# Performance work log

Measured on AMD Instinct MI355X. Metric: run time of the kernel, lower is better.

The kernel has to match this reference:

```python
import jax, jax.numpy as jnp
import numpy as np

N_NODES = 50000
N_EDGES = 1000000
D_NODE = 64
D_EDGE = 64


def setup_inputs() -> dict:
    key = jax.random.key(0)
    ks = jax.random.split(key, 12)
    d, de = D_NODE, D_EDGE
    din = 2 * d + de
    s = lambda f_in: 1.0 / np.sqrt(f_in)
    return {
        "node_feat": jax.random.normal(ks[0], (N_NODES, d), jnp.float32),
        "edge_src": jax.random.randint(ks[1], (N_EDGES,), 0, N_NODES, jnp.int32),
        "edge_dst": jax.random.randint(ks[2], (N_EDGES,), 0, N_NODES, jnp.int32),
        "edge_feat": jax.random.normal(ks[3], (N_EDGES, de), jnp.float32),
        # msg_mlp: Linear(din,d) -> SiLU -> Linear(d,d)
        "W_m1": jax.random.uniform(ks[4], (din, d), jnp.float32, -s(din), s(din)),
        "b_m1": jax.random.uniform(ks[5], (d,), jnp.float32, -s(din), s(din)),
        "W_m2": jax.random.uniform(ks[6], (d, d), jnp.float32, -s(d), s(d)),
        "b_m2": jax.random.uniform(ks[7], (d,), jnp.float32, -s(d), s(d)),
        # update_mlp: Linear(d,d) -> SiLU -> Linear(d,d)
        "W_u1": jax.random.uniform(ks[8], (d, d), jnp.float32, -s(d), s(d)),
        "b_u1": jax.random.uniform(ks[9], (d,), jnp.float32, -s(d), s(d)),
        "W_u2": jax.random.uniform(ks[10], (d, d), jnp.float32, -s(d), s(d)),
        "b_u2": jax.random.uniform(ks[11], (d,), jnp.float32, -s(d), s(d)),
        # LayerNorm params
        "ln_gamma": jnp.ones((d,), jnp.float32),
        "ln_beta": jnp.zeros((d,), jnp.float32),
    }


def _layer_norm(x, gamma, beta, eps=1e-5):
    mu = jnp.mean(x, axis=-1, keepdims=True)
    var = jnp.var(x, axis=-1, keepdims=True)
    return (x - mu) * jax.lax.rsqrt(var + eps) * gamma + beta


def reference(node_feat, edge_src, edge_dst, edge_feat,
              W_m1, b_m1, W_m2, b_m2, W_u1, b_u1, W_u2, b_u2,
              ln_gamma, ln_beta):
    # gather endpoint features per edge: [E, 2d+de]
    msg_input = jnp.concatenate(
        [node_feat[edge_src], node_feat[edge_dst], edge_feat], axis=-1)
    h = jax.nn.silu(msg_input @ W_m1 + b_m1)
    messages = h @ W_m2 + b_m2                      # [E, d]
    aggregated = jax.ops.segment_sum(messages, edge_dst,
                                     num_segments=node_feat.shape[0])
    upd = jax.nn.silu(aggregated @ W_u1 + b_u1) @ W_u2 + b_u2
    return _layer_norm(node_feat + upd, ln_gamma, ln_beta)
```

## Files before the change

kernel.cpp:

```cpp
#include <hip/hip_runtime.h>
#include <stdint.h>

typedef __bf16 bf16;
typedef __attribute__((ext_vector_type(8))) bf16 bf16x8;
typedef __attribute__((ext_vector_type(4))) float f32x4;

#define D 64
#define EPW 32

__device__ __forceinline__ float silu_f(float x) {
    return x / (1.0f + __expf(-x));
}

__global__ void cvt_hist_kernel(const float* __restrict__ nf, bf16* __restrict__ nfb,
                                const int* __restrict__ edst, int* __restrict__ cnt,
                                int total8, int E) {
    const int i = blockIdx.x * blockDim.x + threadIdx.x;
    if (i < total8) {
        f32x4 a = ((const f32x4*)nf)[i*2], b = ((const f32x4*)nf)[i*2 + 1];
        bf16x8 v;
        #pragma unroll
        for (int k = 0; k < 4; ++k) { v[k] = (bf16)a[k]; v[4+k] = (bf16)b[k]; }
        ((bf16x8*)nfb)[i] = v;
    }
    const int stride = gridDim.x * blockDim.x;
    for (int e = i; e < E; e += stride)
        atomicAdd(&cnt[edst[e]], 1);
}

__global__ void scan_part_kernel(const int* __restrict__ cnt, int* __restrict__ part, int N) {
    __shared__ int red[256];
    const int t = threadIdx.x, idx = blockIdx.x * 256 + t;
    red[t] = (idx < N) ? cnt[idx] : 0;
    __syncthreads();
    for (int off = 128; off; off >>= 1) {
        if (t < off) red[t] += red[t + off];
        __syncthreads();
    }
    if (t == 0) part[blockIdx.x] = red[0];
}

__global__ void scan_base_kernel(int* __restrict__ part, int nblk) {
    __shared__ int sc[256];
    const int t = threadIdx.x;
    const int v = (t < nblk) ? part[t] : 0;
    sc[t] = v;
    __syncthreads();
    for (int off = 1; off < 256; off <<= 1) {
        int u = (t >= off) ? sc[t - off] : 0;
        __syncthreads();
        sc[t] += u;
        __syncthreads();
    }
    part[t] = sc[t] - v;
}

__global__ void scan_fin_kernel(const int* __restrict__ cnt, const int* __restrict__ part,
                                int* __restrict__ cur, float* __restrict__ outz, int N) {
    __shared__ int sc[256];
    const int t = threadIdx.x, idx = blockIdx.x * 256 + t;
    const int v = (idx < N) ? cnt[idx] : 0;
    sc[t] = v;
    __syncthreads();
    for (int off = 1; off < 256; off <<= 1) {
        int u = (t >= off) ? sc[t - off] : 0;
        __syncthreads();
        sc[t] += u;
        __syncthreads();
    }
    if (idx < N) {
        cur[idx] = sc[t] - v + part[blockIdx.x];
        f32x4 z = {0.f, 0.f, 0.f, 0.f};
        float* o = outz + (size_t)idx * D;
        #pragma unroll
        for (int i = 0; i < 16; ++i) ((f32x4*)o)[i] = z;
    }
}

__global__ void scatter_kernel(const int* __restrict__ esrc, const int* __restrict__ edst,
                               int* __restrict__ cur, int4* __restrict__ sde, int E) {
    const int stride = gridDim.x * blockDim.x;
    for (int e = blockIdx.x * blockDim.x + threadIdx.x; e < E; e += stride) {
        const int d = edst[e];
        const int pos = atomicAdd(&cur[d], 1);
        sde[pos] = make_int4(esrc[e], d, e, 0);
    }
}

__launch_bounds__(512, 4)
__global__ void mp_edge_sorted_kernel(
    const bf16* __restrict__ nfb,
    const int4* __restrict__ sde,
    const float* __restrict__ efeat,
    const float* __restrict__ W1, const float* __restrict__ b1,
    const float* __restrict__ W2, const float* __restrict__ b2,
    float* __restrict__ agg,
    int E)
{
    __shared__ __align__(16) bf16 W1f[6*4*64*8];
    __shared__ __align__(16) bf16 W2f[2*4*64*8];
    __shared__ __align__(16) bf16 HM[8][32*72];
    __shared__ float b1s[D], b2s[D];

    const int t    = threadIdx.x;
    const int lane = t & 63;
    const int w    = t >> 6;
    const int g    = lane >> 4;
    const int c    = lane & 15;

    for (int idx = t; idx < 6*4*64; idx += 512) {
        int l = idx & 63, nt = (idx >> 6) & 3, ks = idx >> 8;
        int k0 = ks*32 + (l >> 4)*8, col = nt*16 + (l & 15);
        bf16x8 v;
        #pragma unroll
        for (int i = 0; i < 8; ++i) v[i] = (bf16)W1[(k0 + i)*D + col];
        *(bf16x8*)&W1f[idx*8] = v;
    }
    for (int idx = t; idx < 2*4*64; idx += 512) {
        int l = idx & 63, nt = (idx >> 6) & 3, ks = idx >> 8;
        int k0 = ks*32 + (l >> 4)*8, col = nt*16 + (l & 15);
        bf16x8 v;
        #pragma unroll
        for (int i = 0; i < 8; ++i) v[i] = (bf16)W2[(k0 + i)*D + col];
        *(bf16x8*)&W2f[idx*8] = v;
    }
    if (t < D) { b1s[t] = b1[t]; b2s[t] = b2[t]; }
    __syncthreads();

    bf16* hm = &HM[w][0];
    const int nwt = (E + EPW - 1) / EPW;
    const int t0 = blockIdx.x*8 + w;
    const int tstride = gridDim.x*8;

    int4 nq0 = make_int4(0,0,0,0), nq1 = make_int4(0,0,0,0);
    if (t0 < nwt) {
        nq0 = sde[min(t0*EPW + c,      E - 1)];
        nq1 = sde[min(t0*EPW + 16 + c, E - 1)];
    }

    for (int tile = t0; tile < nwt; tile += tstride) {
        const int e0 = tile * EPW;
        const int4 q0 = nq0, q1 = nq1;
        const int tn = tile + tstride;
        if (tn < nwt) {
            nq0 = sde[min(tn*EPW + c,      E - 1)];
            nq1 = sde[min(tn*EPW + 16 + c, E - 1)];
        }
        const int se0 = q0.x, de0 = q0.y, ee0 = q0.z;
        const int se1 = q1.x, de1 = q1.y, ee1 = q1.z;

        f32x4  ef[8];
        #pragma unroll
        for (int ks2 = 0; ks2 < 2; ++ks2) {
            const int coff = ks2*32 + g*8;
            const float* p0 = efeat + (size_t)ee0*D + coff;
            const float* p1 = efeat + (size_t)ee1*D + coff;
            ef[ks2*4+0] = ((const f32x4*)p0)[0];
            ef[ks2*4+1] = ((const f32x4*)p0)[1];
            ef[ks2*4+2] = ((const f32x4*)p1)[0];
            ef[ks2*4+3] = ((const f32x4*)p1)[1];
        }
        bf16x8 an[8];
        #pragma unroll
        for (int ks = 0; ks < 4; ++ks) {
            const int row0 = (ks < 2) ? se0 : de0;
            const int row1 = (ks < 2) ? se1 : de1;
            const int coff = (ks & 1)*32 + g*8;
            an[ks*2]   = *(const bf16x8*)&nfb[(size_t)row0*D + coff];
            an[ks*2+1] = *(const bf16x8*)&nfb[(size_t)row1*D + coff];
        }

        f32x4 acc0[4] = {f32x4{0,0,0,0}, f32x4{0,0,0,0}, f32x4{0,0,0,0}, f32x4{0,0,0,0}};
        f32x4 acc1[4] = {f32x4{0,0,0,0}, f32x4{0,0,0,0}, f32x4{0,0,0,0}, f32x4{0,0,0,0}};
        #pragma unroll
        for (int ks = 0; ks < 4; ++ks) {
            #pragma unroll
            for (int n = 0; n < 4; ++n) {
                bf16x8 bb = *(const bf16x8*)&W1f[((ks*4 + n)*64 + lane)*8];
                acc0[n] = __builtin_amdgcn_mfma_f32_16x16x32_bf16(an[ks*2],   bb, acc0[n], 0, 0, 0);
                acc1[n] = __builtin_amdgcn_mfma_f32_16x16x32_bf16(an[ks*2+1], bb, acc1[n], 0, 0, 0);
            }
        }
        #pragma unroll
        for (int ks2 = 0; ks2 < 2; ++ks2) {
            bf16x8 a0, a1;
            #pragma unroll
            for (int i = 0; i < 4; ++i) {
                a0[i]   = (bf16)ef[ks2*4+0][i];
                a0[4+i] = (bf16)ef[ks2*4+1][i];
                a1[i]   = (bf16)ef[ks2*4+2][i];
                a1[4+i] = (bf16)ef[ks2*4+3][i];
            }
            #pragma unroll
            for (int n = 0; n < 4; ++n) {
                bf16x8 bb = *(const bf16x8*)&W1f[(((ks2+4)*4 + n)*64 + lane)*8];
                acc0[n] = __builtin_amdgcn_mfma_f32_16x16x32_bf16(a0, bb, acc0[n], 0, 0, 0);
                acc1[n] = __builtin_amdgcn_mfma_f32_16x16x32_bf16(a1, bb, acc1[n], 0, 0, 0);
            }
        }

        #pragma unroll
        for (int n = 0; n < 4; ++n) {
            const int col = n*16 + c;
            const float bias = b1s[col];
            #pragma unroll
            for (int j = 0; j < 4; ++j) {
                hm[(g*4 + j)*72 + col]      = (bf16)silu_f(acc0[n][j] + bias);
                hm[(16 + g*4 + j)*72 + col] = (bf16)silu_f(acc1[n][j] + bias);
            }
        }

        f32x4 acc2a[4] = {f32x4{0,0,0,0}, f32x4{0,0,0,0}, f32x4{0,0,0,0}, f32x4{0,0,0,0}};
        f32x4 acc2b[4] = {f32x4{0,0,0,0}, f32x4{0,0,0,0}, f32x4{0,0,0,0}, f32x4{0,0,0,0}};
        #pragma unroll
        for (int ks = 0; ks < 2; ++ks) {
            bf16x8 a0 = *(const bf16x8*)&hm[c*72        + ks*32 + g*8];
            bf16x8 a1 = *(const bf16x8*)&hm[(16 + c)*72 + ks*32 + g*8];
            #pragma unroll
            for (int n = 0; n < 4; ++n) {
                bf16x8 bb = *(const bf16x8*)&W2f[((ks*4 + n)*64 + lane)*8];
                acc2a[n] = __builtin_amdgcn_mfma_f32_16x16x32_bf16(a0, bb, acc2a[n], 0, 0, 0);
                acc2b[n] = __builtin_amdgcn_mfma_f32_16x16x32_bf16(a1, bb, acc2b[n], 0, 0, 0);
            }
        }

        asm volatile("s_waitcnt lgkmcnt(0)" ::: "memory");

        #pragma unroll
        for (int n = 0; n < 4; ++n) {
            const int col = n*16 + c;
            const float bias = b2s[col];
            #pragma unroll
            for (int j = 0; j < 4; ++j) {
                hm[(g*4 + j)*72 + col]      = (bf16)(acc2a[n][j] + bias);
                hm[(16 + g*4 + j)*72 + col] = (bf16)(acc2b[n][j] + bias);
            }
        }

        const int da = __shfl(de0, lane & 15);
        const int db = __shfl(de1, lane & 15);
        const int row = lane & 31;
        int rowd = (lane & 16) ? db : da;
        if (e0 + row >= E) rowd = -1;
        const int prevd = __shfl(rowd, (lane + 63) & 63);
        const bool st = (row == 0) || (rowd != prevd);
        unsigned long long m = __ballot(st) & 0xFFFFFFFFull;

        while (m) {
            const int a = __builtin_ctzll(m); m &= m - 1;
            const int rb = m ? __builtin_ctzll(m) : 32;
            const int d = __shfl(rowd, a);
            if (d >= 0) {
                float s = 0.f;
                for (int r = a; r < rb; ++r) s += (float)hm[r*72 + lane];
                float* dp = &agg[(size_t)d*D + lane];
                if (a > 0 && rb < 32) *dp = s;
                else atomicAdd(dp, s);
            }
        }
    }
}

__launch_bounds__(256, 3)
__global__ void mp_edge_atomic_kernel(
    const float* __restrict__ node_feat,
    const int*   __restrict__ esrc,
    const int*   __restrict__ edst,
    const float* __restrict__ efeat,
    const float* __restrict__ W1, const float* __restrict__ b1,
    const float* __restrict__ W2, const float* __restrict__ b2,
    float* __restrict__ agg,
    int E)
{
    __shared__ __align__(16) bf16 W1f[6*4*64*8];
    __shared__ __align__(16) bf16 W2f[2*4*64*8];
    __shared__ __align__(16) bf16 HM[4][32*72];
    __shared__ float b1s[D], b2s[D];

    const int t    = threadIdx.x;
    const int lane = t & 63;
    const int w    = t >> 6;
    const int g    = lane >> 4;
    const int c    = lane & 15;

    for (int idx = t; idx < 6*4*64; idx += 256) {
        int l = idx & 63, nt = (idx >> 6) & 3, ks = idx >> 8;
        int k0 = ks*32 + (l >> 4)*8, col = nt*16 + (l & 15);
        bf16x8 v;
        #pragma unroll
        for (int i = 0; i < 8; ++i) v[i] = (bf16)W1[(k0 + i)*D + col];
        *(bf16x8*)&W1f[idx*8] = v;
    }
    for (int idx = t; idx < 2*4*64; idx += 256) {
        int l = idx & 63, nt = (idx >> 6) & 3, ks = idx >> 8;
        int k0 = ks*32 + (l >> 4)*8, col = nt*16 + (l & 15);
        bf16x8 v;
        #pragma unroll
        for (int i = 0; i < 8; ++i) v[i] = (bf16)W2[(k0 + i)*D + col];
        *(bf16x8*)&W2f[idx*8] = v;
    }
    if (t < D) { b1s[t] = b1[t]; b2s[t] = b2[t]; }
    __syncthreads();

    bf16* hm = &HM[w][0];
    const int nwt = (E + EPW - 1) / EPW;

    for (int tile = blockIdx.x*4 + w; tile < nwt; tile += gridDim.x*4) {
        const int e0 = tile * EPW;
        const int r0 = min(e0 + c,      E - 1);
        const int r1 = min(e0 + 16 + c, E - 1);
        const int se0 = esrc[r0], de0 = edst[r0];
        const int se1 = esrc[r1], de1 = edst[r1];

        f32x4 acc0[4] = {f32x4{0,0,0,0}, f32x4{0,0,0,0}, f32x4{0,0,0,0}, f32x4{0,0,0,0}};
        f32x4 acc1[4] = {f32x4{0,0,0,0}, f32x4{0,0,0,0}, f32x4{0,0,0,0}, f32x4{0,0,0,0}};
        #pragma unroll
        for (int ks = 0; ks < 6; ++ks) {
            const int col = ks*32 + g*8;
            const float *p0, *p1;
            if (col < 64)       { p0 = node_feat + (size_t)se0*D + col;        p1 = node_feat + (size_t)se1*D + col; }
            else if (col < 128) { p0 = node_feat + (size_t)de0*D + (col - 64); p1 = node_feat + (size_t)de1*D + (col - 64); }
            else                { p0 = efeat + (size_t)r0*D + (col - 128);     p1 = efeat + (size_t)r1*D + (col - 128); }
            f32x4 xa = ((const f32x4*)p0)[0], xb = ((const f32x4*)p0)[1];
            f32x4 ya = ((const f32x4*)p1)[0], yb = ((const f32x4*)p1)[1];
            bf16x8 a0, a1;
            #pragma unroll
            for (int i = 0; i < 4; ++i) {
                a0[i] = (bf16)xa[i];  a0[4+i] = (bf16)xb[i];
                a1[i] = (bf16)ya[i];  a1[4+i] = (bf16)yb[i];
            }
            #pragma unroll
            for (int n = 0; n < 4; ++n) {
                bf16x8 bb = *(const bf16x8*)&W1f[((ks*4 + n)*64 + lane)*8];
                acc0[n] = __builtin_amdgcn_mfma_f32_16x16x32_bf16(a0, bb, acc0[n], 0, 0, 0);
                acc1[n] = __builtin_amdgcn_mfma_f32_16x16x32_bf16(a1, bb, acc1[n], 0, 0, 0);
            }
        }

        #pragma unroll
        for (int n = 0; n < 4; ++n) {
            const int col = n*16 + c;
            const float bias = b1s[col];
            #pragma unroll
            for (int j = 0; j < 4; ++j) {
                hm[(g*4 + j)*72 + col]      = (bf16)silu_f(acc0[n][j] + bias);
                hm[(16 + g*4 + j)*72 + col] = (bf16)silu_f(acc1[n][j] + bias);
            }
        }

        f32x4 acc2a[4] = {f32x4{0,0,0,0}, f32x4{0,0,0,0}, f32x4{0,0,0,0}, f32x4{0,0,0,0}};
        f32x4 acc2b[4] = {f32x4{0,0,0,0}, f32x4{0,0,0,0}, f32x4{0,0,0,0}, f32x4{0,0,0,0}};
        #pragma unroll
        for (int ks = 0; ks < 2; ++ks) {
            bf16x8 a0 = *(const bf16x8*)&hm[c*72        + ks*32 + g*8];
            bf16x8 a1 = *(const bf16x8*)&hm[(16 + c)*72 + ks*32 + g*8];
            #pragma unroll
            for (int n = 0; n < 4; ++n) {
                bf16x8 bb = *(const bf16x8*)&W2f[((ks*4 + n)*64 + lane)*8];
                acc2a[n] = __builtin_amdgcn_mfma_f32_16x16x32_bf16(a0, bb, acc2a[n], 0, 0, 0);
                acc2b[n] = __builtin_amdgcn_mfma_f32_16x16x32_bf16(a1, bb, acc2b[n], 0, 0, 0);
            }
        }

        #pragma unroll
        for (int j = 0; j < 4; ++j) {
            const int row = g*4 + j;
            const int d0 = __shfl(de0, row);
            const int d1 = __shfl(de1, row);
            const bool ok0 = (e0 + row)      < E;
            const bool ok1 = (e0 + 16 + row) < E;
            #pragma unroll
            for (int n = 0; n < 4; ++n) {
                const int col = n*16 + c;
                if (ok0) atomicAdd(&agg[(size_t)d0*D + col], acc2a[n][j] + b2s[col]);
                if (ok1) atomicAdd(&agg[(size_t)d1*D + col], acc2b[n][j] + b2s[col]);
            }
        }
    }
}

__launch_bounds__(256, 4)
__global__ void node_gemm_kernel(
    const float* __restrict__ node_feat,
    const float* __restrict__ Wu1, const float* __restrict__ bu1,
    const float* __restrict__ Wu2, const float* __restrict__ bu2,
    const float* __restrict__ gamma, const float* __restrict__ beta,
    float* __restrict__ inout, int N)
{
    __shared__ __align__(16) bf16 Wf1[2*4*64*8];
    __shared__ __align__(16) bf16 Wf2[2*4*64*8];
    __shared__ __align__(16) bf16 Hs[4][16*72];
    __shared__ float b1s[D], b2s[D], gs[D], bs[D];

    const int t    = threadIdx.x;
    const int lane = t & 63;
    const int w    = t >> 6;
    const int g    = lane >> 4;
    const int c    = lane & 15;

    for (int idx = t; idx < 2*4*64; idx += 256) {
        int l = idx & 63, nt = (idx >> 6) & 3, ks = idx >> 8;
        int k0 = ks*32 + (l >> 4)*8, col = nt*16 + (l & 15);
        bf16x8 v1, v2;
        #pragma unroll
        for (int i = 0; i < 8; ++i) {
            v1[i] = (bf16)Wu1[(k0 + i)*D + col];
            v2[i] = (bf16)Wu2[(k0 + i)*D + col];
        }
        *(bf16x8*)&Wf1[idx*8] = v1;
        *(bf16x8*)&Wf2[idx*8] = v2;
    }
    if (t < D) { b1s[t] = bu1[t]; b2s[t] = bu2[t]; gs[t] = gamma[t]; bs[t] = beta[t]; }
    __syncthreads();

    const int base = blockIdx.x*64 + w*16;
    if (base >= N) return;
    bf16* hs = &Hs[w][0];

    f32x4 acc[4] = {f32x4{0,0,0,0}, f32x4{0,0,0,0}, f32x4{0,0,0,0}, f32x4{0,0,0,0}};
    #pragma unroll
    for (int ks = 0; ks < 2; ++ks) {
        const int rowA = min(base + c, N - 1);
        const float* p = inout + (size_t)rowA*D + ks*32 + g*8;
        f32x4 xa = ((const f32x4*)p)[0], xb = ((const f32x4*)p)[1];
        bf16x8 a;
        #pragma unroll
        for (int i = 0; i < 4; ++i) { a[i] = (bf16)xa[i]; a[4+i] = (bf16)xb[i]; }
        #pragma unroll
        for (int n = 0; n < 4; ++n) {
            bf16x8 bb = *(const bf16x8*)&Wf1[((ks*4 + n)*64 + lane)*8];
            acc[n] = __builtin_amdgcn_mfma_f32_16x16x32_bf16(a, bb, acc[n], 0, 0, 0);
        }
    }
    #pragma unroll
    for (int n = 0; n < 4; ++n) {
        const int col = n*16 + c;
        const float bias = b1s[col];
        #pragma unroll
        for (int j = 0; j < 4; ++j)
            hs[(g*4 + j)*72 + col] = (bf16)silu_f(acc[n][j] + bias);
    }

    f32x4 acc2[4] = {f32x4{0,0,0,0}, f32x4{0,0,0,0}, f32x4{0,0,0,0}, f32x4{0,0,0,0}};
    #pragma unroll
    for (int ks = 0; ks < 2; ++ks) {
        bf16x8 a = *(const bf16x8*)&hs[c*72 + ks*32 + g*8];
        #pragma unroll
        for (int n = 0; n < 4; ++n) {
            bf16x8 bb = *(const bf16x8*)&Wf2[((ks*4 + n)*64 + lane)*8];
            acc2[n] = __builtin_amdgcn_mfma_f32_16x16x32_bf16(a, bb, acc2[n], 0, 0, 0);
        }
    }

    float y[4][4];
    #pragma unroll
    for (int n = 0; n < 4; ++n) {
        const int col = n*16 + c;
        #pragma unroll
        for (int j = 0; j < 4; ++j) {
            const int row = base + g*4 + j;
            const float x0 = (row < N) ? node_feat[(size_t)row*D + col] : 0.f;
            y[n][j] = x0 + acc2[n][j] + b2s[col];
        }
    }
    #pragma unroll
    for (int j = 0; j < 4; ++j) {
        float s1 = 0.f, s2 = 0.f;
        #pragma unroll
        for (int n = 0; n < 4; ++n) { s1 += y[n][j]; s2 += y[n][j]*y[n][j]; }
        #pragma unroll
        for (int mm = 1; mm < 16; mm <<= 1) {
            s1 += __shfl_xor(s1, mm);
            s2 += __shfl_xor(s2, mm);
        }
        const float mu  = s1 * (1.0f/64.0f);
        const float var = s2 * (1.0f/64.0f) - mu*mu;
        const float rs  = rsqrtf(var + 1e-5f);
        const int row = base + g*4 + j;
        if (row < N) {
            #pragma unroll
            for (int n = 0; n < 4; ++n) {
                const int col = n*16 + c;
                inout[(size_t)row*D + col] = (y[n][j] - mu)*rs*gs[col] + bs[col];
            }
        }
    }
}

extern "C" void kernel_launch(void* const* d_in, const int* in_sizes, int n_in,
                              void* d_out, int out_size, void* d_ws, size_t ws_size,
                              hipStream_t stream) {
    const float* node_feat = (const float*)d_in[0];
    const int*   esrc      = (const int*)d_in[1];
    const int*   edst      = (const int*)d_in[2];
    const float* efeat     = (const float*)d_in[3];
    const float* W_m1      = (const float*)d_in[4];
    const float* b_m1      = (const float*)d_in[5];
    const float* W_m2      = (const float*)d_in[6];
    const float* b_m2      = (const float*)d_in[7];
    const float* W_u1      = (const float*)d_in[8];
    const float* b_u1      = (const float*)d_in[9];
    const float* W_u2      = (const float*)d_in[10];
    const float* b_u2      = (const float*)d_in[11];
    const float* ln_gamma  = (const float*)d_in[12];
    const float* ln_beta   = (const float*)d_in[13];

    float* out = (float*)d_out;
    const int E = in_sizes[1];
    const int N = in_sizes[0] / D;

    const size_t sde_bytes = (((size_t)E * 16) + 255) & ~(size_t)255;
    const size_t int_bytes = ((sizeof(int) * (2*(size_t)N + 256)) + 255) & ~(size_t)255;
    const size_t nfb_bytes = (((size_t)N * D * 2) + 255) & ~(size_t)255;
    const size_t need = sde_bytes + int_bytes + nfb_bytes;

    const int nwt    = (E + EPW - 1) / EPW;
    const int gridN  = (N + 63) / 64;
    const int nchunk = (N + 255) / 256;

    if (ws_size >= need) {
        int4* sde  = (int4*)d_ws;
        int*  cnt  = (int*)((char*)d_ws + sde_bytes);
        int*  cur  = cnt + N;
        int*  part = cur + N;
        bf16* nfb  = (bf16*)((char*)d_ws + sde_bytes + int_bytes);

        const int total8 = N * D / 8;
        hipMemsetAsync(cnt, 0, sizeof(int)*(size_t)N, stream);
        cvt_hist_kernel <<<(total8 + 255)/256, 256, 0, stream>>>(node_feat, nfb, edst, cnt, total8, E);
        scan_part_kernel<<<nchunk, 256, 0, stream>>>(cnt, part, N);
        scan_base_kernel<<<1, 256, 0, stream>>>(part, nchunk);
        scan_fin_kernel <<<nchunk, 256, 0, stream>>>(cnt, part, cur, out, N);
        scatter_kernel  <<<1024, 256, 0, stream>>>(esrc, edst, cur, sde, E);

        const int nblk8 = (nwt + 7) / 8;
        const int grid1 = nblk8 < 512 ? nblk8 : 512;
        mp_edge_sorted_kernel<<<grid1, 512, 0, stream>>>(nfb, sde, efeat,
                                                         W_m1, b_m1, W_m2, b_m2,
                                                         out, E);
    } else {
        hipMemsetAsync(out, 0, (size_t)N * D * sizeof(float), stream);
        const int nblk4 = (nwt + 3) / 4;
        const int grid1 = nblk4 < 768 ? nblk4 : 768;
        mp_edge_atomic_kernel<<<grid1, 256, 0, stream>>>(node_feat, esrc, edst, efeat,
                                                         W_m1, b_m1, W_m2, b_m2,
                                                         out, E);
    }

    node_gemm_kernel<<<gridN, 256, 0, stream>>>(node_feat, W_u1, b_u1, W_u2, b_u2,
                                                ln_gamma, ln_beta, out, N);
}
```

Baseline: 244.5 us.

## Replace three-kernel prefix scan with single-block scan and move output zeroing

Collapses the three-pass exclusive scan (partials, base, finalize) into a single 1024-thread block that scans per-thread chunks serially, cutting two kernel launches and their inter-kernel gaps. Zeroing of the output buffer moves into the conversion/histogram kernel. It also reorders the edge kernel so node-feature gathers are issued before edge-feature loads. The single-block scan runs on one CU, with each thread walking about 49 consecutive counts, which could be slower than the multi-block version.

```diff
diff --git a/kernel.cpp b/kernel.cpp
--- a/kernel.cpp
+++ b/kernel.cpp
@@ -14,8 +14,10 @@
 
 __global__ void cvt_hist_kernel(const float* __restrict__ nf, bf16* __restrict__ nfb,
                                 const int* __restrict__ edst, int* __restrict__ cnt,
+                                float* __restrict__ outz,
                                 int total8, int E) {
     const int i = blockIdx.x * blockDim.x + threadIdx.x;
+    const int stride = gridDim.x * blockDim.x;
     if (i < total8) {
         f32x4 a = ((const f32x4*)nf)[i*2], b = ((const f32x4*)nf)[i*2 + 1];
         bf16x8 v;
@@ -23,57 +25,33 @@
         for (int k = 0; k < 4; ++k) { v[k] = (bf16)a[k]; v[4+k] = (bf16)b[k]; }
         ((bf16x8*)nfb)[i] = v;
     }
-    const int stride = gridDim.x * blockDim.x;
+    const f32x4 z = {0.f, 0.f, 0.f, 0.f};
+    const int total4 = total8 * 2;
+    for (int j = i; j < total4; j += stride)
+        ((f32x4*)outz)[j] = z;
     for (int e = i; e < E; e += stride)
         atomicAdd(&cnt[edst[e]], 1);
 }
 
-__global__ void scan_part_kernel(const int* __restrict__ cnt, int* __restrict__ part, int N) {
-    __shared__ int red[256];
-    const int t = threadIdx.x, idx = blockIdx.x * 256 + t;
-    red[t] = (idx < N) ? cnt[idx] : 0;
+__global__ void scan_kernel(const int* __restrict__ cnt, int* __restrict__ cur, int N) {
+    __shared__ int part[1024];
+    const int t  = threadIdx.x;
+    const int CH = (N + 1023) >> 10;
+    const int base = t * CH;
+    int s = 0;
+    for (int i = 0; i < CH; ++i) { int idx = base + i; if (idx < N) s += cnt[idx]; }
+    part[t] = s;
     __syncthreads();
-    for (int off = 128; off; off >>= 1) {
-        if (t < off) red[t] += red[t + off];
+    for (int off = 1; off < 1024; off <<= 1) {
+        int v = (t >= off) ? part[t - off] : 0;
         __syncthreads();
-    }
-    if (t == 0) part[blockIdx.x] = red[0];
-}
-
-__global__ void scan_base_kernel(int* __restrict__ part, int nblk) {
-    __shared__ int sc[256];
-    const int t = threadIdx.x;
-    const int v = (t < nblk) ? part[t] : 0;
-    sc[t] = v;
-    __syncthreads();
-    for (int off = 1; off < 256; off <<= 1) {
-        int u = (t >= off) ? sc[t - off] : 0;
+        part[t] += v;
         __syncthreads();
-        sc[t] += u;
-        __syncthreads();
-    }
-    part[t] = sc[t] - v;
-}
-
-__global__ void scan_fin_kernel(const int* __restrict__ cnt, const int* __restrict__ part,
-                                int* __restrict__ cur, float* __restrict__ outz, int N) {
-    __shared__ int sc[256];
-    const int t = threadIdx.x, idx = blockIdx.x * 256 + t;
-    const int v = (idx < N) ? cnt[idx] : 0;
-    sc[t] = v;
-    __syncthreads();
-    for (int off = 1; off < 256; off <<= 1) {
-        int u = (t >= off) ? sc[t - off] : 0;
-        __syncthreads();
-        sc[t] += u;
-        __syncthreads();
-    }
-    if (idx < N) {
-        cur[idx] = sc[t] - v + part[blockIdx.x];
-        f32x4 z = {0.f, 0.f, 0.f, 0.f};
-        float* o = outz + (size_t)idx * D;
-        #pragma unroll
-        for (int i = 0; i < 16; ++i) ((f32x4*)o)[i] = z;
+    }
+    int run = (t == 0) ? 0 : part[t - 1];
+    for (int i = 0; i < CH; ++i) {
+        int idx = base + i;
+        if (idx < N) { cur[idx] = run; run += cnt[idx]; }
     }
 }
 
@@ -149,7 +127,16 @@
         const int se0 = q0.x, de0 = q0.y, ee0 = q0.z;
         const int se1 = q1.x, de1 = q1.y, ee1 = q1.z;
 
+        bf16x8 an[8];
         f32x4  ef[8];
+        #pragma unroll
+        for (int ks = 0; ks < 4; ++ks) {
+            const int row0 = (ks < 2) ? se0 : de0;
+            const int row1 = (ks < 2) ? se1 : de1;
+            const int coff = (ks & 1)*32 + g*8;
+            an[ks*2]   = *(const bf16x8*)&nfb[(size_t)row0*D + coff];
+            an[ks*2+1] = *(const bf16x8*)&nfb[(size_t)row1*D + coff];
+        }
         #pragma unroll
         for (int ks2 = 0; ks2 < 2; ++ks2) {
             const int coff = ks2*32 + g*8;
@@ -159,15 +146,6 @@
             ef[ks2*4+1] = ((const f32x4*)p0)[1];
             ef[ks2*4+2] = ((const f32x4*)p1)[0];
             ef[ks2*4+3] = ((const f32x4*)p1)[1];
-        }
-        bf16x8 an[8];
-        #pragma unroll
-        for (int ks = 0; ks < 4; ++ks) {
-            const int row0 = (ks < 2) ? se0 : de0;
-            const int row1 = (ks < 2) ? se1 : de1;
-            const int coff = (ks & 1)*32 + g*8;
-            an[ks*2]   = *(const bf16x8*)&nfb[(size_t)row0*D + coff];
-            an[ks*2+1] = *(const bf16x8*)&nfb[(size_t)row1*D + coff];
         }
 
         f32x4 acc0[4] = {f32x4{0,0,0,0}, f32x4{0,0,0,0}, f32x4{0,0,0,0}, f32x4{0,0,0,0}};
@@ -510,28 +488,25 @@
     const int N = in_sizes[0] / D;
 
     const size_t sde_bytes = (((size_t)E * 16) + 255) & ~(size_t)255;
-    const size_t int_bytes = ((sizeof(int) * (2*(size_t)N + 256)) + 255) & ~(size_t)255;
+    const size_t int_bytes = ((sizeof(int) * (2*(size_t)N)) + 255) & ~(size_t)255;
     const size_t nfb_bytes = (((size_t)N * D * 2) + 255) & ~(size_t)255;
     const size_t need = sde_bytes + int_bytes + nfb_bytes;
 
-    const int nwt    = (E + EPW - 1) / EPW;
-    const int gridN  = (N + 63) / 64;
-    const int nchunk = (N + 255) / 256;
+    const int nwt   = (E + EPW - 1) / EPW;
+    const int gridN = (N + 63) / 64;
 
     if (ws_size >= need) {
         int4* sde  = (int4*)d_ws;
         int*  cnt  = (int*)((char*)d_ws + sde_bytes);
         int*  cur  = cnt + N;
-        int*  part = cur + N;
         bf16* nfb  = (bf16*)((char*)d_ws + sde_bytes + int_bytes);
 
         const int total8 = N * D / 8;
         hipMemsetAsync(cnt, 0, sizeof(int)*(size_t)N, stream);
-        cvt_hist_kernel <<<(total8 + 255)/256, 256, 0, stream>>>(node_feat, nfb, edst, cnt, total8, E);
-        scan_part_kernel<<<nchunk, 256, 0, stream>>>(cnt, part, N);
-        scan_base_kernel<<<1, 256, 0, stream>>>(part, nchunk);
-        scan_fin_kernel <<<nchunk, 256, 0, stream>>>(cnt, part, cur, out, N);
-        scatter_kernel  <<<1024, 256, 0, stream>>>(esrc, edst, cur, sde, E);
+        cvt_hist_kernel<<<(total8 + 255)/256, 256, 0, stream>>>(node_feat, nfb, edst, cnt,
+                                                                out, total8, E);
+        scan_kernel    <<<1, 1024, 0, stream>>>(cnt, cur, N);
+        scatter_kernel <<<1024, 256, 0, stream>>>(esrc, edst, cur, sde, E);
 
         const int nblk8 = (nwt + 7) / 8;
         const int grid1 = nblk8 < 512 ? nblk8 : 512;
```

Result: slower. 317.1 us (+29.7%).
